# Kernel optimization log

Hardware: AMD Instinct MI355X
Metric: run time of the kernel (lower is better)

## Reference

```python
import jax, jax.numpy as jnp
import numpy as np

ALPHA = 0.2  # leaky relu slope


def _gat(h, W, b, a_src, a_dst, a_b):
    # h: [B,T,Din]; W: [H,Din,C]; b,a_src,a_dst: [H,C]; a_b: [H]
    Wh = jnp.einsum('btd,hdc->bhtc', h, W) + b[None, :, None, :]
    src = jnp.einsum('bhtc,hc->bht', Wh, a_src)  # score from Wh_i half of concat
    dst = jnp.einsum('bhtc,hc->bht', Wh, a_dst)  # score from Wh_j half
    e = src[:, :, :, None] + dst[:, :, None, :] + a_b[None, :, None, None]  # [B,H,T,T]
    e = jnp.where(e >= 0, e, ALPHA * e)  # leaky_relu
    a = jax.nn.softmax(e, axis=-1)
    out = jnp.einsum('bhij,bhjc->bhic', a, Wh)
    out = jax.nn.relu(out)  # last=False branch
    B, H, T, C = out.shape
    out = out.transpose(0, 2, 1, 3).reshape(B, T, H * C)  # concat heads on feature dim
    return jax.nn.sigmoid(out)


def setup_inputs() -> dict:
    key = jax.random.key(0)
    ks = jax.random.split(key, 15)
    B, T, D = 16, 128, 256
    H, C1, C2, OUT_W = 64, 64, 20, 32
    s = lambda k, shape, fan: jax.random.normal(k, shape, jnp.float32) * (1.0 / np.sqrt(fan))
    return {
        'x': jax.random.normal(ks[0], (B, T, D), jnp.float32),
        'W1': s(ks[1], (H, D, C1), D), 'b1': s(ks[2], (H, C1), D),
        'a1s': s(ks[3], (H, C1), 2 * C1), 'a1d': s(ks[4], (H, C1), 2 * C1),
        'a1b': s(ks[5], (H,), 2 * C1),
        'W2': s(ks[6], (H, H * C1, C2), H * C1), 'b2': s(ks[7], (H, C2), H * C1),
        'a2s': s(ks[8], (H, C2), 2 * C2), 'a2d': s(ks[9], (H, C2), 2 * C2),
        'a2b': s(ks[10], (H,), 2 * C2),
        'sl_w': s(ks[11], (H * C2, D), H * C2), 'sl_b': s(ks[12], (D,), H * C2),
        'gar_w': s(ks[13], (T, OUT_W), T), 'gar_b': s(ks[14], (OUT_W,), T),
    }


def reference(x, W1, b1, a1s, a1d, a1b, W2, b2, a2s, a2d, a2b, sl_w, sl_b, gar_w, gar_b):
    c = _gat(x, W1, b1, a1s, a1d, a1b)          # [B,T,H*C1]
    c = jax.nn.relu(c)
    c = _gat(c, W2, b2, a2s, a2d, a2b)          # [B,T,H*C2]
    c = c @ sl_w + sl_b                          # [B,T,D]
    # GAR: linear over time dim: [B,T,D] -> [B,OUT_W,D]
    res = jnp.einsum('btd,to->bod', c, gar_w) + gar_b[None, :, None]
    return res
```

## Files before the change

### kernel.cpp

```cpp
#include <hip/hip_runtime.h>
#include <hip/hip_bf16.h>

#define B 16
#define T 128
#define D 256
#define H 64
#define C1 64
#define C2 20
#define K2 4096
#define F2 1280
#define OUTW 32
#define ALPHA 0.2f

typedef __attribute__((ext_vector_type(8))) short short8;
typedef __attribute__((ext_vector_type(4))) float f32x4;

static __device__ __forceinline__ ushort f2bf(float f) {
    __hip_bfloat16 h = __float2bfloat16(f);
    return *reinterpret_cast<ushort*>(&h);
}
static __device__ __forceinline__ float bf2f(ushort u) {
    return __uint_as_float(((unsigned int)u) << 16);
}
static __device__ __forceinline__ void gload16(const ushort* g, ushort* l) {
    __builtin_amdgcn_global_load_lds((const unsigned int*)g, (unsigned int*)l,
                                     16, 0, 0);
}

template<int KD, int NBLK, int MBLK, int KSPLIT, int PERM>
__global__ __launch_bounds__(256) void gemm_splitk_kernel(
    const ushort* __restrict__ Ag, const ushort* __restrict__ Bg,
    ushort* __restrict__ Cp)
{
    __shared__ ushort As[128 * 64];
    __shared__ ushort Bs[128 * 64];
    constexpr int NN = NBLK * 128;
    constexpr int MM = MBLK * 128;
    constexpr int NT = MBLK * NBLK;
    constexpr int TOTAL = NT * KSPLIT;
    constexpr int KDP = KD / KSPLIT;
    static_assert(TOTAL % 8 == 0, "swizzle needs multiple of 8 blocks");

    int tid = threadIdx.x;
    int bid = blockIdx.x;
    int wg = (bid & 7) * (TOTAL / 8) + (bid >> 3);
    int kp = wg / NT; int tile = wg - kp * NT;
    int bm = (tile / NBLK) * 128, bn = (tile % NBLK) * 128;

    int wave = tid >> 6, lane = tid & 63;
    int wm = (wave >> 1) * 64, wn = (wave & 1) * 64;
    int lr = lane & 15, lk = lane >> 4;
    int srow = lane >> 3, scol = (lane & 7) * 8;

    f32x4 acc[4][4];
    #pragma unroll
    for (int i = 0; i < 4; ++i)
        #pragma unroll
        for (int j = 0; j < 4; ++j) acc[i][j] = (f32x4){0.f, 0.f, 0.f, 0.f};

    const ushort* ApB = Ag + (size_t)bm * KD + kp * KDP;
    const ushort* BpB = Bg + (size_t)bn * KD + kp * KDP;

    for (int k0 = 0; k0 < KDP; k0 += 64) {
        __syncthreads();
        #pragma unroll
        for (int e = 0; e < 4; ++e) {
            int c = e * 4 + wave;
            gload16(ApB + (size_t)(8 * c + srow) * KD + k0 + scol, &As[c * 512]);
            gload16(BpB + (size_t)(8 * c + srow) * KD + k0 + scol, &Bs[c * 512]);
        }
        __syncthreads();
        #pragma unroll
        for (int ks = 0; ks < 2; ++ks) {
            short8 af[4], bfr[4];
            #pragma unroll
            for (int i = 0; i < 4; ++i)
                af[i] = *(const short8*)&As[(wm + i * 16 + lr) * 64 + ks * 32 + lk * 8];
            #pragma unroll
            for (int j = 0; j < 4; ++j)
                bfr[j] = *(const short8*)&Bs[(wn + j * 16 + lr) * 64 + ks * 32 + lk * 8];
            #pragma unroll
            for (int i = 0; i < 4; ++i)
                #pragma unroll
                for (int j = 0; j < 4; ++j)
                    acc[i][j] = __builtin_amdgcn_mfma_f32_16x16x32_bf16(
                        af[i], bfr[j], acc[i][j], 0, 0, 0);
        }
    }

    if constexpr (PERM) {
        ushort* Cw = Cp + (size_t)kp * MM * NN + (size_t)tile * 16384
                   + wave * 4096 + lane * 4;
        #pragma unroll
        for (int i = 0; i < 4; ++i)
            #pragma unroll
            for (int j = 0; j < 4; ++j) {
                union { ushort q[4]; uint2 v; } pk;
                #pragma unroll
                for (int r = 0; r < 4; ++r) pk.q[r] = f2bf(acc[i][j][r]);
                *(uint2*)&Cw[(i * 4 + j) * 256] = pk.v;
            }
    } else {
        ushort* Cout = Cp + (size_t)kp * MM * NN;
        #pragma unroll
        for (int i = 0; i < 4; ++i) {
            #pragma unroll
            for (int j = 0; j < 4; ++j) {
                int col = bn + wn + j * 16 + lr;
                #pragma unroll
                for (int r = 0; r < 4; ++r) {
                    int row = bm + wm + i * 16 + lk * 4 + r;
                    Cout[(size_t)row * NN + col] = f2bf(acc[i][j][r]);
                }
            }
        }
    }
}

template<int P, int NN>
__global__ __launch_bounds__(256) void reduce_bias_kernel(
    const ushort* __restrict__ parts, const float* __restrict__ bias,
    float* __restrict__ out, int MN)
{
    size_t off = ((size_t)blockIdx.x * 256 + threadIdx.x) * 4;
    float s0 = 0.f, s1 = 0.f, s2 = 0.f, s3 = 0.f;
    #pragma unroll
    for (int p = 0; p < P; ++p) {
        uint2 v = *(const uint2*)&parts[(size_t)p * MN + off];
        s0 += bf2f((ushort)(v.x & 0xffff));
        s1 += bf2f((ushort)(v.x >> 16));
        s2 += bf2f((ushort)(v.y & 0xffff));
        s3 += bf2f((ushort)(v.y >> 16));
    }
    float4 bv = *(const float4*)&bias[(int)(off % NN)];
    float4 o; o.x = s0 + bv.x; o.y = s1 + bv.y; o.z = s2 + bv.z; o.w = s3 + bv.w;
    *(float4*)&out[off] = o;
}

#define WHT_(r,c) whT[(r) * 136 + (c)]

__global__ __launch_bounds__(256) void fused1_kernel(
    const ushort* __restrict__ xbf,
    const ushort* __restrict__ w1t,
    const float* __restrict__ b1,
    const float* __restrict__ a1s, const float* __restrict__ a1d,
    const float* __restrict__ a1b,
    ushort* __restrict__ c1)
{
    int blk = blockIdx.x; int b = blk >> 6, h = blk & 63;
    __shared__ ushort whT[64 * 136];
    __shared__ ushort CT[128 * 72];
    __shared__ float ss[128], ddv[128], sinv[128];

    int tid = threadIdx.x;
    int wave = tid >> 6, lane = tid & 63;
    int wm = (wave >> 1) * 64, wn = (wave & 1) * 32;
    int lr = lane & 15, lk = lane >> 4;

    f32x4 acc[4][2];
    #pragma unroll
    for (int i = 0; i < 4; ++i)
        #pragma unroll
        for (int j = 0; j < 2; ++j) acc[i][j] = (f32x4){0.f, 0.f, 0.f, 0.f};

    const ushort* Abase = xbf + (size_t)(b * T + wm + lr) * D + lk * 8;
    const ushort* Bbase = w1t + (size_t)(h * 64 + wn + lr) * D + lk * 8;

    #pragma unroll 2
    for (int kb = 0; kb < 8; ++kb) {
        short8 af[4], bfr[2];
        #pragma unroll
        for (int i = 0; i < 4; ++i)
            af[i] = *(const short8*)(Abase + (size_t)i * 16 * D + kb * 32);
        #pragma unroll
        for (int j = 0; j < 2; ++j)
            bfr[j] = *(const short8*)(Bbase + (size_t)j * 16 * D + kb * 32);
        #pragma unroll
        for (int i = 0; i < 4; ++i)
            #pragma unroll
            for (int j = 0; j < 2; ++j)
                acc[i][j] = __builtin_amdgcn_mfma_f32_16x16x32_bf16(
                    af[i], bfr[j], acc[i][j], 0, 0, 0);
    }

    #pragma unroll
    for (int j = 0; j < 2; ++j) {
        int col = wn + j * 16 + lr;
        float bv = b1[h * C1 + col];
        #pragma unroll
        for (int i = 0; i < 4; ++i) {
            int t0 = wm + i * 16 + lk * 4;
            union { ushort q[4]; uint2 v; } pk;
            #pragma unroll
            for (int r = 0; r < 4; ++r) pk.q[r] = f2bf(acc[i][j][r] + bv);
            *(uint2*)&WHT_(col, t0) = pk.v;
        }
    }
    __syncthreads();

    {
        int t = tid & 127;
        bool isS = tid < 128;
        const float* av = (isS ? a1s : a1d) + h * C1;
        float s = isS ? a1b[h] : 0.f;
        #pragma unroll 8
        for (int c = 0; c < 64; ++c) s = fmaf(bf2f(WHT_(c, t)), av[c], s);
        if (isS) ss[t] = s; else ddv[t] = s;
    }
    __syncthreads();

    float dm = fmaxf(ddv[lane], ddv[lane + 64]);
    #pragma unroll
    for (int msk = 1; msk < 64; msk <<= 1) dm = fmaxf(dm, __shfl_xor(dm, msk));

    float si[4], mi[4], rsum[4];
    #pragma unroll
    for (int i = 0; i < 4; ++i) {
        si[i] = ss[wm + i * 16 + lr];
        float mx = si[i] + dm;
        mi[i] = mx >= 0.f ? mx : ALPHA * mx;
        rsum[i] = 0.f;
    }

    f32x4 acc2[4][2];
    #pragma unroll
    for (int i = 0; i < 4; ++i)
        #pragma unroll
        for (int j = 0; j < 2; ++j) acc2[i][j] = (f32x4){0.f, 0.f, 0.f, 0.f};

    #pragma unroll
    for (int ks = 0; ks < 4; ++ks) {
        float dj[8];
        #pragma unroll
        for (int e = 0; e < 8; ++e) dj[e] = ddv[ks * 32 + lk * 8 + e];
        short8 bfr[2];
        #pragma unroll
        for (int j = 0; j < 2; ++j)
            bfr[j] = *(const short8*)&WHT_(wn + j * 16 + lr, ks * 32 + lk * 8);
        #pragma unroll
        for (int i = 0; i < 4; ++i) {
            union { ushort q[8]; short8 s; } pk;
            #pragma unroll
            for (int e = 0; e < 8; ++e) {
                float ee = si[i] + dj[e];
                ee = ee >= 0.f ? ee : ALPHA * ee;
                float pp = __expf(ee - mi[i]);
                rsum[i] += pp;
                pk.q[e] = f2bf(pp);
            }
            #pragma unroll
            for (int j = 0; j < 2; ++j)
                acc2[i][j] = __builtin_amdgcn_mfma_f32_16x16x32_bf16(
                    pk.s, bfr[j], acc2[i][j], 0, 0, 0);
        }
    }

    #pragma unroll
    for (int i = 0; i < 4; ++i) {
        rsum[i] += __shfl_xor(rsum[i], 16);
        rsum[i] += __shfl_xor(rsum[i], 32);
    }
    if (lk == 0) {
        #pragma unroll
        for (int i = 0; i < 4; ++i) sinv[wm + i * 16 + lr] = 1.0f / rsum[i];
    }
    __syncthreads();

    #pragma unroll
    for (int i = 0; i < 4; ++i) {
        #pragma unroll
        for (int r = 0; r < 4; ++r) {
            int row = wm + i * 16 + lk * 4 + r;
            float sv = sinv[row];
            #pragma unroll
            for (int j = 0; j < 2; ++j) {
                int col = wn + j * 16 + lr;
                float v = acc2[i][j][r] * sv;
                v = v > 0.f ? v : 0.f;
                v = 1.0f / (1.0f + __expf(-v));
                CT[row * 72 + col] = f2bf(v);
            }
        }
    }
    __syncthreads();
    #pragma unroll
    for (int e = 0; e < 4; ++e) {
        int idx = e * 256 + tid;
        int row = idx >> 3, q = idx & 7;
        uint4 v = *(const uint4*)&CT[row * 72 + q * 8];
        *(uint4*)&c1[((size_t)(b * T + row)) * K2 + h * C1 + q * 8] = v;
    }
}

#define PB2_(r,c)  Pb2[(r) * 136 + (c)]
#define WHT2_(r,c) whT2[(r) * 136 + (c)]

__global__ __launch_bounds__(256) void fused2_kernel(
    const ushort* __restrict__ wh2pb,
    const float* __restrict__ b2,
    const float* __restrict__ a2s, const float* __restrict__ a2d,
    const float* __restrict__ a2b,
    ushort* __restrict__ c2)
{
    int blk = blockIdx.x; int b = blk >> 6, h = blk & 63;
    __shared__ ushort Pb2[128 * 136];
    __shared__ ushort whT2[32 * 136];
    __shared__ float ss[128], ddv[128], sinv[128];

    int tid = threadIdx.x;
    int wave = tid >> 6, lane = tid & 63;
    int lr = lane & 15, lk = lane >> 4;
    const size_t MNfull = (size_t)2048 * F2;

    for (int e = 0; e < 10; ++e) {
        int idx = e * 256 + tid;
        int t = idx / 20, c = idx - t * 20;
        int col = h * C2 + c;
        int tn = col >> 7, cl = col & 127;
        int wv = ((t >> 6) << 1) | (cl >> 6);
        int fi = (t >> 4) & 3, fk = (t >> 2) & 3, fr = t & 3;
        int fj = (cl >> 4) & 3, fl = cl & 15;
        size_t fa = (size_t)(b * 10 + tn) * 16384 + wv * 4096
                  + (fi * 4 + fj) * 256 + (fk * 16 + fl) * 4 + fr;
        float s = b2[col];
        #pragma unroll
        for (int p = 0; p < 8; ++p) s += bf2f(wh2pb[p * MNfull + fa]);
        WHT2_(c, t) = f2bf(s);
    }
    {
        int idx = tid;
        for (int e = 0; e < 6; ++e, idx += 256) {
            int c = 20 + (idx >> 7), t = idx & 127;
            WHT2_(c, t) = 0;
        }
    }
    __syncthreads();

    {
        int t = tid & 127;
        bool isS = tid < 128;
        const float* av = (isS ? a2s : a2d) + h * C2;
        float s = isS ? a2b[h] : 0.f;
        #pragma unroll
        for (int c = 0; c < 20; ++c) s = fmaf(bf2f(WHT2_(c, t)), av[c], s);
        if (isS) ss[t] = s; else ddv[t] = s;
    }
    __syncthreads();

    {
        float dm = fmaxf(ddv[lane], ddv[lane + 64]);
        #pragma unroll
        for (int msk = 1; msk < 64; msk <<= 1) dm = fmaxf(dm, __shfl_xor(dm, msk));
        int i = tid >> 1, j0 = (tid & 1) * 64;
        float si = ss[i];
        float mx = si + dm; mx = mx >= 0.f ? mx : ALPHA * mx;
        float lsum = 0.f;
        #pragma unroll
        for (int g = 0; g < 8; ++g) {
            union { ushort q[8]; uint4 v; } pk;
            #pragma unroll
            for (int e = 0; e < 8; ++e) {
                float ee = si + ddv[j0 + g * 8 + e];
                ee = ee >= 0.f ? ee : ALPHA * ee;
                float pp = __expf(ee - mx);
                lsum += pp;
                pk.q[e] = f2bf(pp);
            }
            *(uint4*)&PB2_(i, j0 + g * 8) = pk.v;
        }
        lsum += __shfl_xor(lsum, 1);
        if (!(tid & 1)) sinv[i] = 1.0f / lsum;
    }
    __syncthreads();

    int wm2 = wave * 32;
    f32x4 acc2[2][2];
    #pragma unroll
    for (int i = 0; i < 2; ++i)
        #pragma unroll
        for (int j = 0; j < 2; ++j) acc2[i][j] = (f32x4){0.f, 0.f, 0.f, 0.f};

    #pragma unroll
    for (int ks = 0; ks < 4; ++ks) {
        short8 af[2], bfr[2];
        #pragma unroll
        for (int i = 0; i < 2; ++i)
            af[i] = *(const short8*)&PB2_(wm2 + i * 16 + lr, ks * 32 + lk * 8);
        #pragma unroll
        for (int j = 0; j < 2; ++j)
            bfr[j] = *(const short8*)&WHT2_(j * 16 + lr, ks * 32 + lk * 8);
        #pragma unroll
        for (int i = 0; i < 2; ++i)
            #pragma unroll
            for (int j = 0; j < 2; ++j)
                acc2[i][j] = __builtin_amdgcn_mfma_f32_16x16x32_bf16(
                    af[i], bfr[j], acc2[i][j], 0, 0, 0);
    }

    __syncthreads();
    ushort* CT2 = Pb2;
    #pragma unroll
    for (int i = 0; i < 2; ++i) {
        #pragma unroll
        for (int r = 0; r < 4; ++r) {
            int row = wm2 + i * 16 + lk * 4 + r;
            float sv = sinv[row];
            #pragma unroll
            for (int j = 0; j < 2; ++j) {
                int col = j * 16 + lr;
                if (col < C2) {
                    float v = acc2[i][j][r] * sv;
                    v = v > 0.f ? v : 0.f;
                    v = 1.0f / (1.0f + __expf(-v));
                    CT2[row * 24 + col] = f2bf(v);
                }
            }
        }
    }
    __syncthreads();
    for (int e = 0; e < 3; ++e) {
        int idx = e * 256 + tid;
        if (idx < 640) {
            int row = idx / 5, q = idx - row * 5;
            uint2 v = *(const uint2*)&CT2[row * 24 + q * 4];
            *(uint2*)&c2[((size_t)(b * T + row)) * F2 + h * C2 + q * 4] = v;
        }
    }
}

__global__ __launch_bounds__(256) void xbf_kernel(
    const float* __restrict__ x, ushort* __restrict__ xbf)
{
    int i = blockIdx.x * 256 + threadIdx.x;
    float4 v = *(const float4*)&x[(size_t)i * 4];
    union { ushort u[4]; uint2 p; } o;
    o.u[0] = f2bf(v.x); o.u[1] = f2bf(v.y);
    o.u[2] = f2bf(v.z); o.u[3] = f2bf(v.w);
    *(uint2*)&xbf[(size_t)i * 4] = o.p;
}

__global__ __launch_bounds__(256) void w1t_kernel(
    const float* __restrict__ W1, ushort* __restrict__ w1t)
{
    int blk = blockIdx.x; int h = blk >> 2, d0 = (blk & 3) * 64;
    __shared__ float lw[64][65];
    int tid = threadIdx.x;
    for (int e = 0; e < 16; ++e) {
        int idx = e * 256 + tid; int dr = idx >> 6, c = idx & 63;
        lw[dr][c] = W1[((size_t)h * D + d0 + dr) * C1 + c];
    }
    __syncthreads();
    for (int e = 0; e < 16; ++e) {
        int idx = e * 256 + tid; int c = idx >> 6, dr = idx & 63;
        w1t[((size_t)(h * 64 + c)) * D + d0 + dr] = f2bf(lw[dr][c]);
    }
}

__global__ __launch_bounds__(256) void w2t_kernel(
    const float* __restrict__ W2, ushort* __restrict__ w2t)
{
    int blk = blockIdx.x; int h = blk >> 5, kb = blk & 31; int k0 = kb * 128;
    __shared__ float lw[128][21];
    int tid = threadIdx.x;
    const float* src = W2 + ((size_t)h * K2 + k0) * C2;
    for (int e = 0; e < 10; ++e) {
        int idx = e * 256 + tid; int k = idx / 20, c = idx - k * 20;
        lw[k][c] = src[idx];
    }
    __syncthreads();
    for (int e = 0; e < 10; ++e) {
        int idx = e * 256 + tid; int c = idx >> 7, k = idx & 127;
        w2t[((size_t)(h * 20 + c)) * K2 + k0 + k] = f2bf(lw[k][c]);
    }
}

__global__ __launch_bounds__(256) void slwt_kernel(
    const float* __restrict__ slw, ushort* __restrict__ slwt)
{
    int blk = blockIdx.x; int kb = blk >> 2, d0 = (blk & 3) * 64; int k0 = kb * 64;
    __shared__ float lw[64][65];
    int tid = threadIdx.x;
    for (int e = 0; e < 16; ++e) {
        int idx = e * 256 + tid; int kr = idx >> 6, dc = idx & 63;
        lw[kr][dc] = slw[((size_t)(k0 + kr)) * D + d0 + dc];
    }
    __syncthreads();
    for (int e = 0; e < 16; ++e) {
        int idx = e * 256 + tid; int dr = idx >> 6, kc = idx & 63;
        slwt[((size_t)(d0 + dr)) * F2 + k0 + kc] = f2bf(lw[kc][dr]);
    }
}

__global__ __launch_bounds__(256) void gar_kernel(
    const float* __restrict__ c3, const float* __restrict__ garw,
    const float* __restrict__ garb, float* __restrict__ out)
{
    int blk = blockIdx.x; int b = blk >> 5, o = blk & 31;
    int dcol = threadIdx.x;
    float acc = garb[o];
    const float* cp = c3 + (size_t)b * T * D + dcol;
    for (int t = 0; t < T; ++t)
        acc = fmaf(cp[(size_t)t * D], garw[t * OUTW + o], acc);
    out[((size_t)b * OUTW + o) * D + dcol] = acc;
}

extern "C" void kernel_launch(void* const* d_in, const int* in_sizes, int n_in,
                              void* d_out, int out_size, void* d_ws, size_t ws_size,
                              hipStream_t stream) {
    const float* x    = (const float*)d_in[0];
    const float* W1   = (const float*)d_in[1];
    const float* b1   = (const float*)d_in[2];
    const float* a1s  = (const float*)d_in[3];
    const float* a1d  = (const float*)d_in[4];
    const float* a1b  = (const float*)d_in[5];
    const float* W2   = (const float*)d_in[6];
    const float* b2   = (const float*)d_in[7];
    const float* a2s  = (const float*)d_in[8];
    const float* a2d  = (const float*)d_in[9];
    const float* a2b  = (const float*)d_in[10];
    const float* slw  = (const float*)d_in[11];
    const float* slb  = (const float*)d_in[12];
    const float* garw = (const float*)d_in[13];
    const float* garb = (const float*)d_in[14];

    char* p = (char*)d_ws;
    float*  c3    = (float*)p;   p += (size_t)2048 * 256  * 4;
    ushort* xbf   = (ushort*)p;  p += (size_t)2048 * 256  * 2;
    ushort* w1t   = (ushort*)p;  p += (size_t)4096 * 256  * 2;
    ushort* c1bf  = (ushort*)p;  p += (size_t)2048 * 4096 * 2;
    ushort* w2t   = (ushort*)p;  p += (size_t)1280 * 4096 * 2;
    ushort* c2bf  = (ushort*)p;  p += (size_t)2048 * 1280 * 2;
    ushort* slwt  = (ushort*)p;  p += (size_t)256  * 1280 * 2;
    ushort* wh2pb = (ushort*)p;  p += (size_t)8 * 2048 * 1280 * 2;
    ushort* c3pb  = (ushort*)c1bf;

    xbf_kernel <<<512,  256, 0, stream>>>(x, xbf);
    w1t_kernel <<<256,  256, 0, stream>>>(W1, w1t);
    w2t_kernel <<<2048, 256, 0, stream>>>(W2, w2t);
    slwt_kernel<<<80,   256, 0, stream>>>(slw, slwt);

    fused1_kernel<<<B * H, 256, 0, stream>>>(xbf, w1t, b1, a1s, a1d, a1b, c1bf);

    gemm_splitk_kernel<4096, 10, 16, 8, 1><<<1280, 256, 0, stream>>>(c1bf, w2t,
                                                                     wh2pb);
    fused2_kernel<<<B * H, 256, 0, stream>>>(wh2pb, b2, a2s, a2d, a2b, c2bf);

    gemm_splitk_kernel<1280, 2, 16, 4, 0><<<128, 256, 0, stream>>>(c2bf, slwt,
                                                                   c3pb);
    reduce_bias_kernel<4, 256><<<512, 256, 0, stream>>>(c3pb, slb, c3, 2048 * 256);

    gar_kernel<<<B * OUTW, 256, 0, stream>>>(c3, garw, garb, (float*)d_out);
}
```

Baseline: 133.3 us.

## Retile fused1 warps to 32x64 and vectorize fused2 split-K partial reduction

In fused1, each wave now computes a 32-row by 64-column tile instead of 64 by 32. This changes A/B fragment reuse and gives each wave all head channels in the attention MFMA stage. In fused2, the split-K partial sums are read four timesteps at a time with 8-byte loads instead of scalar 2-byte loads, which cuts load instructions and index math. The packed layout (fr as the innermost index) makes four consecutive t contiguous, but fewer threads are active in that loop.

```diff
diff --git a/kernel.cpp b/kernel.cpp
--- a/kernel.cpp
+++ b/kernel.cpp
@@ -154,42 +154,42 @@
 
     int tid = threadIdx.x;
     int wave = tid >> 6, lane = tid & 63;
-    int wm = (wave >> 1) * 64, wn = (wave & 1) * 32;
+    int wm2 = wave * 32;
     int lr = lane & 15, lk = lane >> 4;
 
-    f32x4 acc[4][2];
-    #pragma unroll
-    for (int i = 0; i < 4; ++i)
-        #pragma unroll
-        for (int j = 0; j < 2; ++j) acc[i][j] = (f32x4){0.f, 0.f, 0.f, 0.f};
-
-    const ushort* Abase = xbf + (size_t)(b * T + wm + lr) * D + lk * 8;
-    const ushort* Bbase = w1t + (size_t)(h * 64 + wn + lr) * D + lk * 8;
+    f32x4 acc[2][4];
+    #pragma unroll
+    for (int i = 0; i < 2; ++i)
+        #pragma unroll
+        for (int j = 0; j < 4; ++j) acc[i][j] = (f32x4){0.f, 0.f, 0.f, 0.f};
+
+    const ushort* Abase = xbf + (size_t)(b * T + wm2 + lr) * D + lk * 8;
+    const ushort* Bbase = w1t + (size_t)(h * 64 + lr) * D + lk * 8;
 
     #pragma unroll 2
     for (int kb = 0; kb < 8; ++kb) {
-        short8 af[4], bfr[2];
-        #pragma unroll
-        for (int i = 0; i < 4; ++i)
+        short8 af[2], bfr[4];
+        #pragma unroll
+        for (int i = 0; i < 2; ++i)
             af[i] = *(const short8*)(Abase + (size_t)i * 16 * D + kb * 32);
         #pragma unroll
-        for (int j = 0; j < 2; ++j)
+        for (int j = 0; j < 4; ++j)
             bfr[j] = *(const short8*)(Bbase + (size_t)j * 16 * D + kb * 32);
         #pragma unroll
-        for (int i = 0; i < 4; ++i)
-            #pragma unroll
-            for (int j = 0; j < 2; ++j)
+        for (int i = 0; i < 2; ++i)
+            #pragma unroll
+            for (int j = 0; j < 4; ++j)
                 acc[i][j] = __builtin_amdgcn_mfma_f32_16x16x32_bf16(
                     af[i], bfr[j], acc[i][j], 0, 0, 0);
     }
 
     #pragma unroll
-    for (int j = 0; j < 2; ++j) {
-        int col = wn + j * 16 + lr;
+    for (int j = 0; j < 4; ++j) {
+        int col = j * 16 + lr;
         float bv = b1[h * C1 + col];
         #pragma unroll
-        for (int i = 0; i < 4; ++i) {
-            int t0 = wm + i * 16 + lk * 4;
+        for (int i = 0; i < 2; ++i) {
+            int t0 = wm2 + i * 16 + lk * 4;
             union { ushort q[4]; uint2 v; } pk;
             #pragma unroll
             for (int r = 0; r < 4; ++r) pk.q[r] = f2bf(acc[i][j][r] + bv);
@@ -213,32 +213,32 @@
     #pragma unroll
     for (int msk = 1; msk < 64; msk <<= 1) dm = fmaxf(dm, __shfl_xor(dm, msk));
 
-    float si[4], mi[4], rsum[4];
-    #pragma unroll
-    for (int i = 0; i < 4; ++i) {
-        si[i] = ss[wm + i * 16 + lr];
+    float si[2], mi[2], rsum[2];
+    #pragma unroll
+    for (int i = 0; i < 2; ++i) {
+        si[i] = ss[wm2 + i * 16 + lr];
         float mx = si[i] + dm;
         mi[i] = mx >= 0.f ? mx : ALPHA * mx;
         rsum[i] = 0.f;
     }
 
-    f32x4 acc2[4][2];
-    #pragma unroll
-    for (int i = 0; i < 4; ++i)
-        #pragma unroll
-        for (int j = 0; j < 2; ++j) acc2[i][j] = (f32x4){0.f, 0.f, 0.f, 0.f};
+    f32x4 acc2[2][4];
+    #pragma unroll
+    for (int i = 0; i < 2; ++i)
+        #pragma unroll
+        for (int j = 0; j < 4; ++j) acc2[i][j] = (f32x4){0.f, 0.f, 0.f, 0.f};
 
     #pragma unroll
     for (int ks = 0; ks < 4; ++ks) {
         float dj[8];
         #pragma unroll
         for (int e = 0; e < 8; ++e) dj[e] = ddv[ks * 32 + lk * 8 + e];
-        short8 bfr[2];
-        #pragma unroll
-        for (int j = 0; j < 2; ++j)
-            bfr[j] = *(const short8*)&WHT_(wn + j * 16 + lr, ks * 32 + lk * 8);
-        #pragma unroll
-        for (int i = 0; i < 4; ++i) {
+        short8 bfr[4];
+        #pragma unroll
+        for (int j = 0; j < 4; ++j)
+            bfr[j] = *(const short8*)&WHT_(j * 16 + lr, ks * 32 + lk * 8);
+        #pragma unroll
+        for (int i = 0; i < 2; ++i) {
             union { ushort q[8]; short8 s; } pk;
             #pragma unroll
             for (int e = 0; e < 8; ++e) {
@@ -249,32 +249,32 @@
                 pk.q[e] = f2bf(pp);
             }
             #pragma unroll
-            for (int j = 0; j < 2; ++j)
+            for (int j = 0; j < 4; ++j)
                 acc2[i][j] = __builtin_amdgcn_mfma_f32_16x16x32_bf16(
                     pk.s, bfr[j], acc2[i][j], 0, 0, 0);
         }
     }
 
     #pragma unroll
-    for (int i = 0; i < 4; ++i) {
+    for (int i = 0; i < 2; ++i) {
         rsum[i] += __shfl_xor(rsum[i], 16);
         rsum[i] += __shfl_xor(rsum[i], 32);
     }
     if (lk == 0) {
         #pragma unroll
-        for (int i = 0; i < 4; ++i) sinv[wm + i * 16 + lr] = 1.0f / rsum[i];
-    }
-    __syncthreads();
-
-    #pragma unroll
-    for (int i = 0; i < 4; ++i) {
+        for (int i = 0; i < 2; ++i) sinv[wm2 + i * 16 + lr] = 1.0f / rsum[i];
+    }
+    __syncthreads();
+
+    #pragma unroll
+    for (int i = 0; i < 2; ++i) {
         #pragma unroll
         for (int r = 0; r < 4; ++r) {
-            int row = wm + i * 16 + lk * 4 + r;
+            int row = wm2 + i * 16 + lk * 4 + r;
             float sv = sinv[row];
             #pragma unroll
-            for (int j = 0; j < 2; ++j) {
-                int col = wn + j * 16 + lr;
+            for (int j = 0; j < 4; ++j) {
+                int col = j * 16 + lr;
                 float v = acc2[i][j][r] * sv;
                 v = v > 0.f ? v : 0.f;
                 v = 1.0f / (1.0f + __expf(-v));
@@ -312,20 +312,33 @@
     int lr = lane & 15, lk = lane >> 4;
     const size_t MNfull = (size_t)2048 * F2;
 
-    for (int e = 0; e < 10; ++e) {
+    for (int e = 0; e < 3; ++e) {
         int idx = e * 256 + tid;
-        int t = idx / 20, c = idx - t * 20;
-        int col = h * C2 + c;
-        int tn = col >> 7, cl = col & 127;
-        int wv = ((t >> 6) << 1) | (cl >> 6);
-        int fi = (t >> 4) & 3, fk = (t >> 2) & 3, fr = t & 3;
-        int fj = (cl >> 4) & 3, fl = cl & 15;
-        size_t fa = (size_t)(b * 10 + tn) * 16384 + wv * 4096
-                  + (fi * 4 + fj) * 256 + (fk * 16 + fl) * 4 + fr;
-        float s = b2[col];
-        #pragma unroll
-        for (int p = 0; p < 8; ++p) s += bf2f(wh2pb[p * MNfull + fa]);
-        WHT2_(c, t) = f2bf(s);
+        if (idx < 640) {
+            int tq = idx / 20, c = idx - tq * 20;
+            int col = h * C2 + c;
+            int tn = col >> 7, cl = col & 127;
+            int fj = (cl >> 4) & 3, fl = cl & 15;
+            int t0 = tq * 4;
+            int wv = ((t0 >> 6) << 1) | (cl >> 6);
+            int fi = (t0 >> 4) & 3, fk = (t0 >> 2) & 3;
+            size_t fa = (size_t)(b * 10 + tn) * 16384 + wv * 4096
+                      + (fi * 4 + fj) * 256 + (fk * 16 + fl) * 4;
+            float bv = b2[col];
+            float s0 = bv, s1 = bv, s2 = bv, s3 = bv;
+            #pragma unroll
+            for (int p = 0; p < 8; ++p) {
+                uint2 v = *(const uint2*)&wh2pb[p * MNfull + fa];
+                s0 += bf2f((ushort)(v.x & 0xffff));
+                s1 += bf2f((ushort)(v.x >> 16));
+                s2 += bf2f((ushort)(v.y & 0xffff));
+                s3 += bf2f((ushort)(v.y >> 16));
+            }
+            union { ushort q[4]; uint2 u; } o;
+            o.q[0] = f2bf(s0); o.q[1] = f2bf(s1);
+            o.q[2] = f2bf(s2); o.q[3] = f2bf(s3);
+            *(uint2*)&WHT2_(c, t0) = o.u;
+        }
     }
     {
         int idx = tid;
```

Result: faster. 124.1 us (-6.9%).
